# Performance work log

Hardware: AMD Instinct MI355X
Metric: run time of the kernel (lower is better)

## Reference

```python
import jax, jax.numpy as jnp
import numpy as np

TEMPERATURE = 0.1
EPS = 1e-08
NEG_INF = -9e15


def setup_inputs() -> dict:
    key = jax.random.key(0)
    k1, k2 = jax.random.split(key)
    B, D = 4096, 256
    z_i = jax.random.normal(k1, (B, D), dtype=jnp.float32)
    z_j = jax.random.normal(k2, (B, D), dtype=jnp.float32)
    mask_positive = jnp.ones((B,), dtype=bool)
    return {"z_i": z_i, "z_j": z_j, "mask_positive": mask_positive}


def reference(z_i, z_j, mask_positive):
    B = z_i.shape[0]
    N = 2 * B
    z = jnp.concatenate([z_i, z_j], axis=0)  # [N, D]
    # cosine similarity: normalize (norms clamped to eps) then GEMM
    norms = jnp.maximum(jnp.linalg.norm(z, axis=1, keepdims=True), EPS)
    zn = z / norms
    sim = jnp.matmul(zn, zn.T) / TEMPERATURE  # [N, N]
    # mask self-similarity on diagonal
    rows = jnp.arange(N)
    sim = sim.at[rows, rows].set(NEG_INF)
    logprob = jax.nn.log_softmax(sim, axis=1)
    # positive of row k is row (k+B) mod N
    positives = jnp.concatenate([jnp.arange(B, N), jnp.arange(0, B)])
    loss_vec = -logprob[rows, positives]  # [N]
    mp = jnp.concatenate([mask_positive, mask_positive])  # [N] bool
    cnt = jnp.sum(mp.astype(jnp.float32))
    total = jnp.sum(jnp.where(mp, loss_vec, 0.0))
    loss = jnp.where(cnt > 0, total / jnp.maximum(cnt, 1.0), 0.0)
    return loss
```

## Files before the change

### kernel.cpp

```cpp
#include <hip/hip_runtime.h>
#include <hip/hip_bf16.h>

#define NTOT   8192
#define BHALF  4096
#define DDIM   256
#define SMOD   16
#define NPART  4
#define MAXSLOT 9
#define EXPSCALE 14.4269504088896341f

typedef __attribute__((ext_vector_type(8))) short bf16x8_t;
typedef __attribute__((ext_vector_type(4))) float f32x4_t;

__device__ inline unsigned short f2bf(float x) {
    __hip_bfloat16 h = __float2bfloat16(x);
    return __builtin_bit_cast(unsigned short, h);
}

__global__ void norm_pair_kernel(const float* __restrict__ zi,
                                 const float* __restrict__ zj,
                                 unsigned short* __restrict__ zn,
                                 float* __restrict__ posdot,
                                 float* __restrict__ s_part) {
    int gtid = blockIdx.x * 256 + threadIdx.x;
    if (gtid < NTOT * NPART) s_part[gtid] = 0.0f;
    int k    = gtid >> 6;
    int lane = gtid & 63;
    float4 vi = reinterpret_cast<const float4*>(zi + (size_t)k * DDIM)[lane];
    float4 vj = reinterpret_cast<const float4*>(zj + (size_t)k * DDIM)[lane];
    float ssi = vi.x*vi.x + vi.y*vi.y + vi.z*vi.z + vi.w*vi.w;
    float ssj = vj.x*vj.x + vj.y*vj.y + vj.z*vj.z + vj.w*vj.w;
    float dot = vi.x*vj.x + vi.y*vj.y + vi.z*vj.z + vi.w*vj.w;
    #pragma unroll
    for (int off = 32; off >= 1; off >>= 1) {
        ssi += __shfl_xor(ssi, off);
        ssj += __shfl_xor(ssj, off);
        dot += __shfl_xor(dot, off);
    }
    float ri = 1.0f / fmaxf(sqrtf(ssi), 1e-8f);
    float rj = 1.0f / fmaxf(sqrtf(ssj), 1e-8f);
    ushort4 oi, oj;
    oi.x = f2bf(vi.x * ri); oi.y = f2bf(vi.y * ri);
    oi.z = f2bf(vi.z * ri); oi.w = f2bf(vi.w * ri);
    oj.x = f2bf(vj.x * rj); oj.y = f2bf(vj.y * rj);
    oj.z = f2bf(vj.z * rj); oj.w = f2bf(vj.w * rj);
    reinterpret_cast<ushort4*>(zn + (size_t)k * DDIM)[lane] = oi;
    reinterpret_cast<ushort4*>(zn + (size_t)(k + BHALF) * DDIM)[lane] = oj;
    if (lane == 0) posdot[k] = dot * ri * rj * 10.0f;
}

__global__ void __launch_bounds__(256, 2)
gemm_sym_kernel(const unsigned short* __restrict__ zn,
                float* __restrict__ s_part) {
    __shared__ unsigned short ldsB[64 * 256];
    __shared__ float colLDS[MAXSLOT][4][64];

    const int tid  = threadIdx.x;
    const int lane = tid & 63;
    const int wv   = tid >> 6;
    const int m    = lane & 15;
    const int quad = lane >> 4;
    const int biA  = blockIdx.x;
    const int s    = blockIdx.y;

    float* rowPart = s_part + (size_t)(s   & (NPART - 1)) * NTOT;
    float* colPart = s_part + (size_t)(biA & (NPART - 1)) * NTOT;

    int slot = 0;
    #pragma unroll
    for (int p = 0; p < 2; ++p) {
        const int bi = p ? (63 - biA) : biA;
        const int R0 = bi << 7;
        const int cs0 = 2 * bi + ((s - 2 * bi) & (SMOD - 1));
        if (cs0 >= 128) continue;

        bf16x8_t afrag[2][8];
        #pragma unroll
        for (int rf = 0; rf < 2; ++rf) {
            const unsigned short* arow = zn + (size_t)(R0 + wv*32 + rf*16 + m) * DDIM;
            #pragma unroll
            for (int kk = 0; kk < 8; ++kk)
                afrag[rf][kk] = *reinterpret_cast<const bf16x8_t*>(arow + kk*32 + quad*8);
        }

        float rowacc[2][4] = {{0.f,0.f,0.f,0.f},{0.f,0.f,0.f,0.f}};

        for (int cs = cs0; cs < 128; cs += SMOD) {
            const int C0 = cs << 6;
            const bool isDiag = ((cs >> 1) == bi);

            __syncthreads();
            #pragma unroll
            for (int t = 0; t < 8; ++t) {
                int ci = t * 256 + tid;
                int r = ci >> 5, c = ci & 31;
                bf16x8_t v = *reinterpret_cast<const bf16x8_t*>(
                                 zn + (size_t)(C0 + r) * DDIM + c * 8);
                *reinterpret_cast<bf16x8_t*>(&ldsB[r * 256 + ((c ^ (r & 7)) << 3)]) = v;
            }
            __syncthreads();

            #pragma unroll
            for (int cf = 0; cf < 4; ++cf) {
                f32x4_t c0 = (f32x4_t){0.f,0.f,0.f,0.f};
                f32x4_t c1 = (f32x4_t){0.f,0.f,0.f,0.f};
                #pragma unroll
                for (int kk = 0; kk < 8; ++kk) {
                    bf16x8_t b = *reinterpret_cast<const bf16x8_t*>(
                        &ldsB[(cf*16 + m) * 256 + (((kk*4 + quad) ^ (m & 7)) << 3)]);
                    c0 = __builtin_amdgcn_mfma_f32_16x16x32_bf16(afrag[0][kk], b, c0, 0, 0, 0);
                    c1 = __builtin_amdgcn_mfma_f32_16x16x32_bf16(afrag[1][kk], b, c1, 0, 0, 0);
                }
                const int gc = C0 + cf*16 + m;
                float colsum = 0.f;
                #pragma unroll
                for (int r = 0; r < 4; ++r) {
                    int gr0 = R0 + wv*32 + quad*4 + r;
                    float e0 = exp2f(c0[r] * EXPSCALE);
                    float e1 = exp2f(c1[r] * EXPSCALE);
                    if (isDiag && gr0 == gc)        e0 = 0.f;
                    if (isDiag && (gr0 + 16) == gc) e1 = 0.f;
                    rowacc[0][r] += e0;
                    rowacc[1][r] += e1;
                    colsum += e0 + e1;
                }
                if (!isDiag) {
                    colsum += __shfl_xor(colsum, 16);
                    colsum += __shfl_xor(colsum, 32);
                    if (quad == 0) colLDS[slot][wv][cf*16 + m] = colsum;
                }
            }
            ++slot;
        }

        #pragma unroll
        for (int rf = 0; rf < 2; ++rf)
            #pragma unroll
            for (int r = 0; r < 4; ++r) {
                float v = rowacc[rf][r];
                v += __shfl_xor(v, 1);
                v += __shfl_xor(v, 2);
                v += __shfl_xor(v, 4);
                v += __shfl_xor(v, 8);
                if (m == 0)
                    atomicAdd(&rowPart[R0 + wv*32 + rf*16 + quad*4 + r], v);
            }
    }

    __syncthreads();

    if (tid < 64) {
        int slot2 = 0;
        #pragma unroll
        for (int p = 0; p < 2; ++p) {
            const int bi = p ? (63 - biA) : biA;
            const int cs0 = 2 * bi + ((s - 2 * bi) & (SMOD - 1));
            if (cs0 >= 128) continue;
            for (int cs = cs0; cs < 128; cs += SMOD) {
                if ((cs >> 1) != bi) {
                    float v = colLDS[slot2][0][tid] + colLDS[slot2][1][tid]
                            + colLDS[slot2][2][tid] + colLDS[slot2][3][tid];
                    atomicAdd(&colPart[(cs << 6) + tid], v);
                }
                ++slot2;
            }
        }
    }
}

__global__ void finalize_kernel(const float* __restrict__ s_part,
                                const float* __restrict__ posdot,
                                const unsigned char* __restrict__ mask,
                                float* __restrict__ out) {
    int tid = threadIdx.x, lane = tid & 63, wv = tid >> 6;
    float tot = 0.f, cnt = 0.f;
    #pragma unroll
    for (int si = 0; si < NTOT / 1024; ++si) {
        int k = si * 1024 + tid;
        int kb = k & (BHALF - 1);
        if (mask[kb] != 0) {
            float sk = s_part[k] + s_part[NTOT + k]
                     + s_part[2*NTOT + k] + s_part[3*NTOT + k];
            tot += __logf(sk) - posdot[kb];
            cnt += 1.f;
        }
    }
    #pragma unroll
    for (int off = 32; off >= 1; off >>= 1) {
        tot += __shfl_xor(tot, off);
        cnt += __shfl_xor(cnt, off);
    }
    __shared__ float st[16], sc[16];
    if (lane == 0) { st[wv] = tot; sc[wv] = cnt; }
    __syncthreads();
    if (tid == 0) {
        float T = 0.f, C = 0.f;
        #pragma unroll
        for (int i = 0; i < 16; ++i) { T += st[i]; C += sc[i]; }
        out[0] = (C > 0.f) ? (T / fmaxf(C, 1.f)) : 0.f;
    }
}

extern "C" void kernel_launch(void* const* d_in, const int* in_sizes, int n_in,
                              void* d_out, int out_size, void* d_ws, size_t ws_size,
                              hipStream_t stream) {
    const float* zi = (const float*)d_in[0];
    const float* zj = (const float*)d_in[1];
    const unsigned char* mask = (const unsigned char*)d_in[2];
    float* out = (float*)d_out;

    unsigned short* zn = (unsigned short*)d_ws;
    float* s_part = (float*)((char*)d_ws + (size_t)NTOT * DDIM * 2);
    float* posdot = s_part + NPART * NTOT;

    norm_pair_kernel<<<dim3(1024), dim3(256), 0, stream>>>(zi, zj, zn, posdot, s_part);
    gemm_sym_kernel<<<dim3(32, SMOD), dim3(256), 0, stream>>>(zn, s_part);
    finalize_kernel<<<dim3(1), dim3(1024), 0, stream>>>(s_part, posdot, mask, out);
}
```

Measured before the change: 107.8 us.

## Double-buffer B tile with direct global-to-LDS loads in symmetric GEMM

Replaces the register-staged copy of each 64-column B tile into LDS with direct global-to-LDS loads, applying the XOR swizzle on the global side so the LDS layout stays the same. The tile buffer is doubled so the next tile is prefetched while the current one feeds the MFMAs, which leaves one barrier per iteration instead of two. The aim is to hide global load latency behind compute. In exchange LDS use doubles to about 64KB plus colLDS, which may limit the two-blocks-per-CU target, and the manual waitcnt and barrier ordering is fragile.

```diff
diff --git a/kernel.cpp b/kernel.cpp
--- a/kernel.cpp
+++ b/kernel.cpp
@@ -52,7 +52,7 @@
 __global__ void __launch_bounds__(256, 2)
 gemm_sym_kernel(const unsigned short* __restrict__ zn,
                 float* __restrict__ s_part) {
-    __shared__ unsigned short ldsB[64 * 256];
+    __shared__ unsigned short ldsB[2][64 * 256];
     __shared__ float colLDS[MAXSLOT][4][64];
 
     const int tid  = threadIdx.x;
@@ -66,6 +66,9 @@
     float* rowPart = s_part + (size_t)(s   & (NPART - 1)) * NTOT;
     float* colPart = s_part + (size_t)(biA & (NPART - 1)) * NTOT;
 
+    const int sr = tid >> 5;
+    const int sc = tid & 31;
+
     int slot = 0;
     #pragma unroll
     for (int p = 0; p < 2; ++p) {
@@ -85,21 +88,47 @@
 
         float rowacc[2][4] = {{0.f,0.f,0.f,0.f},{0.f,0.f,0.f,0.f}};
 
+        {
+            const int C0 = cs0 << 6;
+            #pragma unroll
+            for (int t = 0; t < 8; ++t) {
+                const int r = t * 8 + sr;
+                const unsigned short* g =
+                    zn + (size_t)(C0 + r) * DDIM + ((sc ^ (r & 7)) << 3);
+                __builtin_amdgcn_global_load_lds(
+                    (const __attribute__((address_space(1))) unsigned int*)g,
+                    (__attribute__((address_space(3))) unsigned int*)
+                        &ldsB[0][(t * 256 + tid) * 8],
+                    16, 0, 0);
+            }
+        }
+
+        int cur = 0;
         for (int cs = cs0; cs < 128; cs += SMOD) {
             const int C0 = cs << 6;
             const bool isDiag = ((cs >> 1) == bi);
 
-            __syncthreads();
-            #pragma unroll
-            for (int t = 0; t < 8; ++t) {
-                int ci = t * 256 + tid;
-                int r = ci >> 5, c = ci & 31;
-                bf16x8_t v = *reinterpret_cast<const bf16x8_t*>(
-                                 zn + (size_t)(C0 + r) * DDIM + c * 8);
-                *reinterpret_cast<bf16x8_t*>(&ldsB[r * 256 + ((c ^ (r & 7)) << 3)]) = v;
-            }
-            __syncthreads();
-
+            asm volatile("s_waitcnt vmcnt(0)" ::: "memory");
+            __builtin_amdgcn_s_barrier();
+            __builtin_amdgcn_sched_barrier(0);
+
+            if (cs + SMOD < 128) {
+                const int C1 = (cs + SMOD) << 6;
+                unsigned short* dst = ldsB[cur ^ 1];
+                #pragma unroll
+                for (int t = 0; t < 8; ++t) {
+                    const int r = t * 8 + sr;
+                    const unsigned short* g =
+                        zn + (size_t)(C1 + r) * DDIM + ((sc ^ (r & 7)) << 3);
+                    __builtin_amdgcn_global_load_lds(
+                        (const __attribute__((address_space(1))) unsigned int*)g,
+                        (__attribute__((address_space(3))) unsigned int*)
+                            (dst + (t * 256 + tid) * 8),
+                        16, 0, 0);
+                }
+            }
+
+            const unsigned short* Bt = ldsB[cur];
             #pragma unroll
             for (int cf = 0; cf < 4; ++cf) {
                 f32x4_t c0 = (f32x4_t){0.f,0.f,0.f,0.f};
@@ -107,7 +136,7 @@
                 #pragma unroll
                 for (int kk = 0; kk < 8; ++kk) {
                     bf16x8_t b = *reinterpret_cast<const bf16x8_t*>(
-                        &ldsB[(cf*16 + m) * 256 + (((kk*4 + quad) ^ (m & 7)) << 3)]);
+                        Bt + (cf*16 + m) * 256 + (((kk*4 + quad) ^ (m & 7)) << 3));
                     c0 = __builtin_amdgcn_mfma_f32_16x16x32_bf16(afrag[0][kk], b, c0, 0, 0, 0);
                     c1 = __builtin_amdgcn_mfma_f32_16x16x32_bf16(afrag[1][kk], b, c1, 0, 0, 0);
                 }
@@ -130,6 +159,7 @@
                     if (quad == 0) colLDS[slot][wv][cf*16 + m] = colsum;
                 }
             }
+            cur ^= 1;
             ++slot;
         }
 
@@ -145,9 +175,14 @@
                 if (m == 0)
                     atomicAdd(&rowPart[R0 + wv*32 + rf*16 + quad*4 + r], v);
             }
-    }
-
-    __syncthreads();
+
+        __builtin_amdgcn_s_barrier();
+        __builtin_amdgcn_sched_barrier(0);
+    }
+
+    asm volatile("s_waitcnt lgkmcnt(0)" ::: "memory");
+    __builtin_amdgcn_s_barrier();
+    __builtin_amdgcn_sched_barrier(0);
 
     if (tid < 64) {
         int slot2 = 0;
```

Measured after the change: 105.7 us. About the same (-1.9%).

## Make each wave an independent 32-row tile, dropping LDS staging and block syncs

Applied to the files above, without the earlier changes.

The symmetric GEMM work is redistributed so that each wave owns a 32-row strip and its own strided set of 64-column tiles. B fragments are loaded straight from global memory into registers instead of being staged through swizzled LDS, which removes the __syncthreads barriers and the colLDS buffer. Column sums are now atomically added per wave rather than after a block-level reduction. The diagonal-tile masking becomes a strict upper-triangle mask. The trade-off is more global/L2 traffic, since B tiles are no longer shared across the four waves, plus four times as many column atomics.

```diff
diff --git a/kernel.cpp b/kernel.cpp
--- a/kernel.cpp
+++ b/kernel.cpp
@@ -4,9 +4,7 @@
 #define NTOT   8192
 #define BHALF  4096
 #define DDIM   256
-#define SMOD   16
 #define NPART  4
-#define MAXSLOT 9
 #define EXPSCALE 14.4269504088896341f
 
 typedef __attribute__((ext_vector_type(8))) short bf16x8_t;
@@ -52,85 +50,93 @@
 __global__ void __launch_bounds__(256, 2)
 gemm_sym_kernel(const unsigned short* __restrict__ zn,
                 float* __restrict__ s_part) {
-    __shared__ unsigned short ldsB[64 * 256];
-    __shared__ float colLDS[MAXSLOT][4][64];
-
     const int tid  = threadIdx.x;
     const int lane = tid & 63;
     const int wv   = tid >> 6;
     const int m    = lane & 15;
     const int quad = lane >> 4;
-    const int biA  = blockIdx.x;
-    const int s    = blockIdx.y;
-
-    float* rowPart = s_part + (size_t)(s   & (NPART - 1)) * NTOT;
-    float* colPart = s_part + (size_t)(biA & (NPART - 1)) * NTOT;
-
-    int slot = 0;
-    #pragma unroll
-    for (int p = 0; p < 2; ++p) {
-        const int bi = p ? (63 - biA) : biA;
-        const int R0 = bi << 7;
-        const int cs0 = 2 * bi + ((s - 2 * bi) & (SMOD - 1));
-        if (cs0 >= 128) continue;
+    const int wid  = blockIdx.x * 4 + wv;
+    const int p    = wid >> 4;
+    const int j    = wid & 15;
+
+    float* rowPart = s_part + (size_t)(j & (NPART - 1)) * NTOT;
+    float* colPart = s_part + (size_t)(p & (NPART - 1)) * NTOT;
+
+    #pragma unroll
+    for (int phase = 0; phase < 2; ++phase) {
+        const int R  = phase ? (255 - p) : p;
+        const int b  = R >> 1;
+        const int jj = phase ? (15 - j) : j;
+        int C = b + ((jj - b) & 15);
+        if (C >= 128) continue;
 
         bf16x8_t afrag[2][8];
         #pragma unroll
         for (int rf = 0; rf < 2; ++rf) {
-            const unsigned short* arow = zn + (size_t)(R0 + wv*32 + rf*16 + m) * DDIM;
+            const unsigned short* arow =
+                zn + (size_t)((R << 5) + rf*16 + m) * DDIM + quad*8;
             #pragma unroll
             for (int kk = 0; kk < 8; ++kk)
-                afrag[rf][kk] = *reinterpret_cast<const bf16x8_t*>(arow + kk*32 + quad*8);
+                afrag[rf][kk] = *reinterpret_cast<const bf16x8_t*>(arow + kk*32);
         }
 
         float rowacc[2][4] = {{0.f,0.f,0.f,0.f},{0.f,0.f,0.f,0.f}};
 
-        for (int cs = cs0; cs < 128; cs += SMOD) {
-            const int C0 = cs << 6;
-            const bool isDiag = ((cs >> 1) == bi);
-
-            __syncthreads();
-            #pragma unroll
-            for (int t = 0; t < 8; ++t) {
-                int ci = t * 256 + tid;
-                int r = ci >> 5, c = ci & 31;
-                bf16x8_t v = *reinterpret_cast<const bf16x8_t*>(
-                                 zn + (size_t)(C0 + r) * DDIM + c * 8);
-                *reinterpret_cast<bf16x8_t*>(&ldsB[r * 256 + ((c ^ (r & 7)) << 3)]) = v;
-            }
-            __syncthreads();
+        for (; C < 128; C += 16) {
+            const bool diag = (C == b);
+            const int C0 = C << 6;
+
+            f32x4_t acc[2][4];
+            #pragma unroll
+            for (int rf = 0; rf < 2; ++rf)
+                #pragma unroll
+                for (int cf = 0; cf < 4; ++cf)
+                    acc[rf][cf] = (f32x4_t){0.f,0.f,0.f,0.f};
 
             #pragma unroll
             for (int cf = 0; cf < 4; ++cf) {
-                f32x4_t c0 = (f32x4_t){0.f,0.f,0.f,0.f};
-                f32x4_t c1 = (f32x4_t){0.f,0.f,0.f,0.f};
+                const unsigned short* brow =
+                    zn + (size_t)(C0 + cf*16 + m) * DDIM + quad*8;
+                bf16x8_t bfr[8];
+                #pragma unroll
+                for (int kk = 0; kk < 8; ++kk)
+                    bfr[kk] = *reinterpret_cast<const bf16x8_t*>(brow + kk*32);
                 #pragma unroll
                 for (int kk = 0; kk < 8; ++kk) {
-                    bf16x8_t b = *reinterpret_cast<const bf16x8_t*>(
-                        &ldsB[(cf*16 + m) * 256 + (((kk*4 + quad) ^ (m & 7)) << 3)]);
-                    c0 = __builtin_amdgcn_mfma_f32_16x16x32_bf16(afrag[0][kk], b, c0, 0, 0, 0);
-                    c1 = __builtin_amdgcn_mfma_f32_16x16x32_bf16(afrag[1][kk], b, c1, 0, 0, 0);
+                    acc[0][cf] = __builtin_amdgcn_mfma_f32_16x16x32_bf16(
+                                     afrag[0][kk], bfr[kk], acc[0][cf], 0, 0, 0);
+                    acc[1][cf] = __builtin_amdgcn_mfma_f32_16x16x32_bf16(
+                                     afrag[1][kk], bfr[kk], acc[1][cf], 0, 0, 0);
                 }
+            }
+
+            float colsum[4] = {0.f, 0.f, 0.f, 0.f};
+            #pragma unroll
+            for (int cf = 0; cf < 4; ++cf) {
                 const int gc = C0 + cf*16 + m;
-                float colsum = 0.f;
-                #pragma unroll
-                for (int r = 0; r < 4; ++r) {
-                    int gr0 = R0 + wv*32 + quad*4 + r;
-                    float e0 = exp2f(c0[r] * EXPSCALE);
-                    float e1 = exp2f(c1[r] * EXPSCALE);
-                    if (isDiag && gr0 == gc)        e0 = 0.f;
-                    if (isDiag && (gr0 + 16) == gc) e1 = 0.f;
-                    rowacc[0][r] += e0;
-                    rowacc[1][r] += e1;
-                    colsum += e0 + e1;
-                }
-                if (!isDiag) {
-                    colsum += __shfl_xor(colsum, 16);
-                    colsum += __shfl_xor(colsum, 32);
-                    if (quad == 0) colLDS[slot][wv][cf*16 + m] = colsum;
-                }
-            }
-            ++slot;
+                #pragma unroll
+                for (int rf = 0; rf < 2; ++rf)
+                    #pragma unroll
+                    for (int r = 0; r < 4; ++r) {
+                        float e = exp2f(acc[rf][cf][r] * EXPSCALE);
+                        if (diag) {
+                            int gr = (R << 5) + rf*16 + quad*4 + r;
+                            e = (gc > gr) ? e : 0.f;
+                        }
+                        rowacc[rf][r] += e;
+                        colsum[cf]    += e;
+                    }
+            }
+            #pragma unroll
+            for (int cf = 0; cf < 4; ++cf) {
+                colsum[cf] += __shfl_xor(colsum[cf], 16);
+                colsum[cf] += __shfl_xor(colsum[cf], 32);
+            }
+            float v = colsum[0];
+            v = (quad == 1) ? colsum[1] : v;
+            v = (quad == 2) ? colsum[2] : v;
+            v = (quad == 3) ? colsum[3] : v;
+            atomicAdd(&colPart[C0 + lane], v);
         }
 
         #pragma unroll
@@ -143,28 +149,8 @@
                 v += __shfl_xor(v, 4);
                 v += __shfl_xor(v, 8);
                 if (m == 0)
-                    atomicAdd(&rowPart[R0 + wv*32 + rf*16 + quad*4 + r], v);
-            }
-    }
-
-    __syncthreads();
-
-    if (tid < 64) {
-        int slot2 = 0;
-        #pragma unroll
-        for (int p = 0; p < 2; ++p) {
-            const int bi = p ? (63 - biA) : biA;
-            const int cs0 = 2 * bi + ((s - 2 * bi) & (SMOD - 1));
-            if (cs0 >= 128) continue;
-            for (int cs = cs0; cs < 128; cs += SMOD) {
-                if ((cs >> 1) != bi) {
-                    float v = colLDS[slot2][0][tid] + colLDS[slot2][1][tid]
-                            + colLDS[slot2][2][tid] + colLDS[slot2][3][tid];
-                    atomicAdd(&colPart[(cs << 6) + tid], v);
-                }
-                ++slot2;
-            }
-        }
+                    atomicAdd(&rowPart[(R << 5) + rf*16 + quad*4 + r], v);
+            }
     }
 }
 
@@ -214,6 +200,6 @@
     float* posdot = s_part + NPART * NTOT;
 
     norm_pair_kernel<<<dim3(1024), dim3(256), 0, stream>>>(zi, zj, zn, posdot, s_part);
-    gemm_sym_kernel<<<dim3(32, SMOD), dim3(256), 0, stream>>>(zn, s_part);
+    gemm_sym_kernel<<<dim3(512), dim3(256), 0, stream>>>(zn, s_part);
     finalize_kernel<<<dim3(1), dim3(1024), 0, stream>>>(s_part, posdot, mask, out);
 }
```

New measurement: 145.0 us. 1.35x slower.

## Double-buffer B tile via direct global-to-LDS loads interleaved with MFMA

Applied to the files above, without the earlier changes.

Doubles the LDS B buffer and uses global_load_lds to stream the next column tile directly into shared memory while the current tile is consumed, with loads split across the four cf sub-steps. B fragments are now read into registers before the MFMA chain, and explicit barriers plus sched_barrier and setprio control ordering. The intent is to hide global-load latency behind compute. In exchange it doubles LDS use, which may hurt occupancy, and adds extra barriers per sub-step whose ordering around the async LDS writes must be correct.

```diff
diff --git a/kernel.cpp b/kernel.cpp
--- a/kernel.cpp
+++ b/kernel.cpp
@@ -52,7 +52,7 @@
 __global__ void __launch_bounds__(256, 2)
 gemm_sym_kernel(const unsigned short* __restrict__ zn,
                 float* __restrict__ s_part) {
-    __shared__ unsigned short ldsB[64 * 256];
+    __shared__ unsigned short ldsB[2][64 * 256];
     __shared__ float colLDS[MAXSLOT][4][64];
 
     const int tid  = threadIdx.x;
@@ -66,6 +66,20 @@
     float* rowPart = s_part + (size_t)(s   & (NPART - 1)) * NTOT;
     float* colPart = s_part + (size_t)(biA & (NPART - 1)) * NTOT;
 
+#define STAGE2(dst, C1, t0) {                                                 \
+    _Pragma("unroll")                                                         \
+    for (int t_ = (t0); t_ < (t0) + 2; ++t_) {                                \
+        int ci_ = t_ * 256 + tid;                                             \
+        int r_ = ci_ >> 5, c_ = ci_ & 31;                                     \
+        const unsigned short* g_ =                                            \
+            zn + (size_t)((C1) + r_) * DDIM + ((c_ ^ (r_ & 7)) << 3);         \
+        __builtin_amdgcn_global_load_lds(                                     \
+            (const __attribute__((address_space(1))) unsigned int*)g_,        \
+            (__attribute__((address_space(3))) unsigned int*)                 \
+                ((dst) + (size_t)ci_ * 8),                                    \
+            16, 0, 0);                                                        \
+    } }
+
     int slot = 0;
     #pragma unroll
     for (int p = 0; p < 2; ++p) {
@@ -85,32 +99,46 @@
 
         float rowacc[2][4] = {{0.f,0.f,0.f,0.f},{0.f,0.f,0.f,0.f}};
 
+        STAGE2(ldsB[0], cs0 << 6, 0);
+        STAGE2(ldsB[0], cs0 << 6, 2);
+        STAGE2(ldsB[0], cs0 << 6, 4);
+        STAGE2(ldsB[0], cs0 << 6, 6);
+
+        int cur = 0;
         for (int cs = cs0; cs < 128; cs += SMOD) {
             const int C0 = cs << 6;
-            const bool isDiag = ((cs >> 1) == bi);
-
-            __syncthreads();
-            #pragma unroll
-            for (int t = 0; t < 8; ++t) {
-                int ci = t * 256 + tid;
-                int r = ci >> 5, c = ci & 31;
-                bf16x8_t v = *reinterpret_cast<const bf16x8_t*>(
-                                 zn + (size_t)(C0 + r) * DDIM + c * 8);
-                *reinterpret_cast<bf16x8_t*>(&ldsB[r * 256 + ((c ^ (r & 7)) << 3)]) = v;
-            }
-            __syncthreads();
+            const bool isDiag  = ((cs >> 1) == bi);
+            const bool haveNxt = (cs + SMOD < 128);
+            const int  C1      = (cs + SMOD) << 6;
+            unsigned short* nxt = ldsB[cur ^ 1];
+            const unsigned short* Bt = ldsB[cur];
+
+            asm volatile("s_waitcnt vmcnt(0)" ::: "memory");
+            __builtin_amdgcn_s_barrier();
+            __builtin_amdgcn_sched_barrier(0);
 
             #pragma unroll
             for (int cf = 0; cf < 4; ++cf) {
+                bf16x8_t bfr[8];
+                #pragma unroll
+                for (int kk = 0; kk < 8; ++kk)
+                    bfr[kk] = *reinterpret_cast<const bf16x8_t*>(
+                        Bt + (cf*16 + m) * 256 + (((kk*4 + quad) ^ (m & 7)) << 3));
+                if (haveNxt) STAGE2(nxt, C1, cf * 2);
+                __builtin_amdgcn_sched_barrier(0);
+                __builtin_amdgcn_s_barrier();
+                __builtin_amdgcn_sched_barrier(0);
+
+                __builtin_amdgcn_s_setprio(1);
                 f32x4_t c0 = (f32x4_t){0.f,0.f,0.f,0.f};
                 f32x4_t c1 = (f32x4_t){0.f,0.f,0.f,0.f};
                 #pragma unroll
                 for (int kk = 0; kk < 8; ++kk) {
-                    bf16x8_t b = *reinterpret_cast<const bf16x8_t*>(
-                        &ldsB[(cf*16 + m) * 256 + (((kk*4 + quad) ^ (m & 7)) << 3)]);
-                    c0 = __builtin_amdgcn_mfma_f32_16x16x32_bf16(afrag[0][kk], b, c0, 0, 0, 0);
-                    c1 = __builtin_amdgcn_mfma_f32_16x16x32_bf16(afrag[1][kk], b, c1, 0, 0, 0);
-                }
+                    c0 = __builtin_amdgcn_mfma_f32_16x16x32_bf16(afrag[0][kk], bfr[kk], c0, 0, 0, 0);
+                    c1 = __builtin_amdgcn_mfma_f32_16x16x32_bf16(afrag[1][kk], bfr[kk], c1, 0, 0, 0);
+                }
+                __builtin_amdgcn_s_setprio(0);
+
                 const int gc = C0 + cf*16 + m;
                 float colsum = 0.f;
                 #pragma unroll
@@ -129,7 +157,10 @@
                     colsum += __shfl_xor(colsum, 32);
                     if (quad == 0) colLDS[slot][wv][cf*16 + m] = colsum;
                 }
+                __builtin_amdgcn_sched_barrier(0);
+                __builtin_amdgcn_s_barrier();
             }
+            cur ^= 1;
             ++slot;
         }
 
@@ -145,9 +176,15 @@
                 if (m == 0)
                     atomicAdd(&rowPart[R0 + wv*32 + rf*16 + quad*4 + r], v);
             }
-    }
-
-    __syncthreads();
+
+        __builtin_amdgcn_s_barrier();
+        __builtin_amdgcn_sched_barrier(0);
+    }
+#undef STAGE2
+
+    asm volatile("s_waitcnt lgkmcnt(0)" ::: "memory");
+    __builtin_amdgcn_s_barrier();
+    __builtin_amdgcn_sched_barrier(0);
 
     if (tid < 64) {
         int slot2 = 0;
```

New measurement: 106.7 us. About the same (-1.0%).
